# Performance work log

Hardware: AMD Instinct MI355X
Metric: run time of the kernel (lower is better)

The kernel has to match this reference:

```python
import jax, jax.numpy as jnp
import numpy as np
from jax.ops import segment_sum, segment_max

N = 50000          # nodes
E = 1_600_000      # edges (before self-loops)
IN = 16            # in_channels
F = 20             # N_features
H1 = 4             # heads in conv1
EDGE_DIM = 7
OUT = 3            # out_channels
NEG_SLOPE = 0.2


def setup_inputs() -> dict:
    key = jax.random.key(0)
    ks = jax.random.split(key, 24)
    g = lambda k, shape, fan: (jax.random.normal(k, shape, jnp.float32)
                               * (1.0 / np.sqrt(fan)))
    inp = {}
    inp["x"] = jax.random.normal(ks[0], (N, IN), jnp.float32)
    inp["edge_index"] = jax.random.randint(ks[1], (2, E), 0, N, jnp.int32)
    inp["edge_attr"] = jax.random.normal(ks[2], (E, EDGE_DIM), jnp.float32)
    # conv1: IN -> F, heads=H1, edge_dim=EDGE_DIM
    inp["W1"] = g(ks[3], (IN, H1 * F), IN)
    inp["att_src1"] = g(ks[4], (H1, F), F)
    inp["att_dst1"] = g(ks[5], (H1, F), F)
    inp["We1"] = g(ks[6], (EDGE_DIM, H1 * F), EDGE_DIM)
    inp["att_e1"] = g(ks[7], (H1, F), F)
    inp["b1"] = jnp.zeros((H1 * F,), jnp.float32)
    # conv2: (H1*F) -> F, heads=1, edge_dim=EDGE_DIM
    inp["W2"] = g(ks[8], (H1 * F, F), H1 * F)
    inp["att_src2"] = g(ks[9], (1, F), F)
    inp["att_dst2"] = g(ks[10], (1, F), F)
    inp["We2"] = g(ks[11], (EDGE_DIM, F), EDGE_DIM)
    inp["att_e2"] = g(ks[12], (1, F), F)
    inp["b2"] = jnp.zeros((F,), jnp.float32)
    # decoder: F -> 10 -> OUT
    inp["D1w"] = g(ks[13], (F, 10), F)
    inp["D1b"] = jnp.zeros((10,), jnp.float32)
    inp["D2w"] = g(ks[14], (10, OUT), 10)
    inp["D2b"] = jnp.zeros((OUT,), jnp.float32)
    return inp


def _gat_layer(x, src, dst, eattr, W, a_s, a_d, We, a_e, b, heads, fdim):
    """PyG GATConv (shared src/dst lin, add_self_loops already applied)."""
    n = x.shape[0]
    xh = (x @ W).reshape(n, heads, fdim)                  # [N,H,F]
    eh = (eattr @ We).reshape(-1, heads, fdim)            # [Ea,H,F]
    a_src = jnp.sum(xh * a_s, axis=-1)                    # [N,H]
    a_dst = jnp.sum(xh * a_d, axis=-1)                    # [N,H]
    a_edge = jnp.sum(eh * a_e, axis=-1)                   # [Ea,H]
    logits = a_src[src] + a_dst[dst] + a_edge             # [Ea,H]
    logits = jnp.where(logits >= 0, logits, NEG_SLOPE * logits)
    # segment softmax over destination node
    m = segment_max(logits, dst, num_segments=n)          # [N,H]
    ex = jnp.exp(logits - m[dst])
    denom = segment_sum(ex, dst, num_segments=n)          # [N,H]
    alpha = ex / (denom[dst] + 1e-16)                     # [Ea,H]
    msg = xh[src] * alpha[:, :, None]                     # [Ea,H,F]
    out = segment_sum(msg, dst, num_segments=n)           # [N,H,F]
    return out.reshape(n, heads * fdim) + b


def reference(x, edge_index, edge_attr, W1, att_src1, att_dst1, We1, att_e1,
              b1, W2, att_src2, att_dst2, We2, att_e2, b2, D1w, D1b, D2w, D2b):
    src, dst = edge_index[0], edge_index[1]
    # add self-loops with edge_attr fill_value='mean' (scatter-mean by dst)
    deg = segment_sum(jnp.ones((E,), jnp.float32), dst, num_segments=N)
    mean_attr = segment_sum(edge_attr, dst, num_segments=N) \
        / jnp.maximum(deg, 1.0)[:, None]
    loops = jnp.arange(N, dtype=src.dtype)
    src_a = jnp.concatenate([src, loops])
    dst_a = jnp.concatenate([dst, loops])
    eattr_a = jnp.concatenate([edge_attr, mean_attr], axis=0)
    # conv1 (heads=4, concat) -> elu  (dropouts are no-ops in eval)
    h = _gat_layer(x, src_a, dst_a, eattr_a, W1, att_src1, att_dst1,
                   We1, att_e1, b1, H1, F)
    h = jax.nn.elu(h)
    # conv2 (heads=1) -> elu
    h = _gat_layer(h, src_a, dst_a, eattr_a, W2, att_src2, att_dst2,
                   We2, att_e2, b2, 1, F)
    h = jax.nn.elu(h)
    # decoder MLP
    h = jax.nn.relu(h @ D1w + D1b)
    return h @ D2w + D2b
```

## Files before the change

### kernel.cpp

```cpp
#include <hip/hip_runtime.h>
#include <hip/hip_fp16.h>

constexpr int NN  = 50000;
constexpr int EEg = 1600000;
constexpr int IND = 16;
constexpr int FD  = 20;
constexpr int H1D = 4;
constexpr int ED  = 7;
constexpr int OUTD = 3;
constexpr int FP  = 24;

__device__ __forceinline__ float lrelu(float x) { return x >= 0.0f ? x : 0.2f * x; }
__device__ __forceinline__ float elu(float x)   { return x > 0.0f ? x : expm1f(x); }
__device__ __forceinline__ unsigned pack2(float a, float b) {
    __half2 h = __floats2half2_rn(a, b);
    return *(unsigned*)&h;
}
__device__ __forceinline__ float2 up2(unsigned w) {
    __half2 h = *(__half2*)&w;
    return __half22float2(h);
}

__global__ void k_deg(const int* __restrict__ ei, int* __restrict__ deg,
                      int* __restrict__ rank) {
    int e = blockIdx.x * blockDim.x + threadIdx.x;
    if (e >= EEg) return;
    rank[e] = atomicAdd(&deg[ei[EEg + e]], 1);
}

__global__ void k_ve(const float* __restrict__ We1, const float* __restrict__ ae1,
                     const float* __restrict__ We2, const float* __restrict__ ae2,
                     float* __restrict__ ve1, float* __restrict__ ve2) {
    int t = threadIdx.x;
    if (t < ED * H1D) {
        int d = t >> 2, h = t & 3;
        float s = 0.0f;
        for (int f = 0; f < FD; ++f) s += We1[d * (H1D * FD) + h * FD + f] * ae1[h * FD + f];
        ve1[t] = s;
    } else if (t < ED * H1D + ED) {
        int d = t - ED * H1D;
        float s = 0.0f;
        for (int f = 0; f < FD; ++f) s += We2[d * FD + f] * ae2[f];
        ve2[d] = s;
    }
}

__global__ void k_scanA(const int* __restrict__ deg, int* __restrict__ partial,
                        int* __restrict__ bsum) {
    __shared__ int sd[256];
    int t = threadIdx.x, i = blockIdx.x * 256 + t;
    int v = (i < NN) ? deg[i] : 0;
    sd[t] = v;
    __syncthreads();
    for (int off = 1; off < 256; off <<= 1) {
        int u = (t >= off) ? sd[t - off] : 0;
        __syncthreads();
        sd[t] += u;
        __syncthreads();
    }
    if (i < NN) partial[i] = sd[t] - v;
    if (t == 255) bsum[blockIdx.x] = sd[255];
}
__global__ void k_scanB(const int* __restrict__ bsum, int* __restrict__ boff, int nb) {
    __shared__ int sd[256];
    int t = threadIdx.x;
    int v = (t < nb) ? bsum[t] : 0;
    sd[t] = v;
    __syncthreads();
    for (int off = 1; off < 256; off <<= 1) {
        int u = (t >= off) ? sd[t - off] : 0;
        __syncthreads();
        sd[t] += u;
        __syncthreads();
    }
    if (t < nb) boff[t] = sd[t] - v;
}
__global__ void k_scanC(const int* __restrict__ partial, const int* __restrict__ boff,
                        int* __restrict__ row_off) {
    int i = blockIdx.x * 256 + threadIdx.x;
    if (i < NN) row_off[i] = partial[i] + boff[blockIdx.x];
    if (i == 0) row_off[NN] = EEg;
}

__global__ void k_scatter(const int* __restrict__ ei, const float* __restrict__ eattr,
                          const float* __restrict__ ve1, const float* __restrict__ ve2,
                          const int* __restrict__ row_off, const int* __restrict__ rank,
                          uint4* __restrict__ csr) {
    __shared__ float sv1[ED * H1D], sv2[ED];
    if (threadIdx.x < ED * H1D) sv1[threadIdx.x] = ve1[threadIdx.x];
    if (threadIdx.x < ED) sv2[threadIdx.x] = ve2[threadIdx.x];
    __syncthreads();
    int e = blockIdx.x * blockDim.x + threadIdx.x;
    if (e >= EEg) return;
    int src = ei[e], dst = ei[EEg + e];
    float a[ED];
#pragma unroll
    for (int d = 0; d < ED; ++d) a[d] = eattr[e * ED + d];
    float v0 = 0.f, v1 = 0.f, v2 = 0.f, v3 = 0.f, w2 = 0.f;
#pragma unroll
    for (int d = 0; d < ED; ++d) {
        v0 += a[d] * sv1[d * H1D + 0];
        v1 += a[d] * sv1[d * H1D + 1];
        v2 += a[d] * sv1[d * H1D + 2];
        v3 += a[d] * sv1[d * H1D + 3];
        w2 += a[d] * sv2[d];
    }
    int slot = row_off[dst] + rank[e];
    uint4 rec;
    rec.x = (unsigned)src;
    rec.y = pack2(v0, v1);
    rec.z = pack2(v2, v3);
    rec.w = pack2(w2, 0.0f);
    csr[slot] = rec;
}

__global__ void k_mean_self(const int* __restrict__ row_off, const uint4* __restrict__ csr,
                            float* __restrict__ a_e1s, float* __restrict__ a_e2s) {
    int n = blockIdx.x * blockDim.x + threadIdx.x;
    if (n >= NN) return;
    int beg = row_off[n], end = row_off[n + 1];
    float s0 = 0.f, s1 = 0.f, s2 = 0.f, s3 = 0.f, se = 0.f;
    for (int j = beg; j < end; ++j) {
        uint4 r = csr[j];
        float2 a01 = up2(r.y), a23 = up2(r.z), ap = up2(r.w);
        s0 += a01.x; s1 += a01.y; s2 += a23.x; s3 += a23.y; se += ap.x;
    }
    float inv = 1.0f / fmaxf((float)(end - beg), 1.0f);
    a_e1s[n * H1D + 0] = s0 * inv;
    a_e1s[n * H1D + 1] = s1 * inv;
    a_e1s[n * H1D + 2] = s2 * inv;
    a_e1s[n * H1D + 3] = s3 * inv;
    a_e2s[n] = se * inv;
}

__global__ void k_xh1attn1(const float* __restrict__ x, const float* __restrict__ W1,
                           const float* __restrict__ as, const float* __restrict__ ad,
                           __half* __restrict__ xh1h, float* __restrict__ a_src1,
                           float* __restrict__ a_dst1) {
    __shared__ float sW[IND * H1D * FD];
    for (int i = threadIdx.x; i < IND * H1D * FD; i += blockDim.x) sW[i] = W1[i];
    __syncthreads();
    int idx = blockIdx.x * blockDim.x + threadIdx.x;
    if (idx >= NN * H1D) return;
    int n = idx >> 2, h = idx & 3;
    float xr[IND];
    const float4* xp = (const float4*)&x[(size_t)n * IND];
#pragma unroll
    for (int q = 0; q < IND / 4; ++q) {
        float4 v = xp[q];
        xr[4 * q] = v.x; xr[4 * q + 1] = v.y; xr[4 * q + 2] = v.z; xr[4 * q + 3] = v.w;
    }
    float ss = 0.f, sd = 0.f;
    float o[FD];
#pragma unroll
    for (int f = 0; f < FD; ++f) {
        float s = 0.f;
#pragma unroll
        for (int k = 0; k < IND; ++k) s += xr[k] * sW[k * (H1D * FD) + h * FD + f];
        o[f] = s;
        ss += s * as[h * FD + f];
        sd += s * ad[h * FD + f];
    }
    uint4* xo = (uint4*)&xh1h[((size_t)n * H1D + h) * FP];
    xo[0] = make_uint4(pack2(o[0], o[1]), pack2(o[2], o[3]), pack2(o[4], o[5]), pack2(o[6], o[7]));
    xo[1] = make_uint4(pack2(o[8], o[9]), pack2(o[10], o[11]), pack2(o[12], o[13]), pack2(o[14], o[15]));
    xo[2] = make_uint4(pack2(o[16], o[17]), pack2(o[18], o[19]), 0u, 0u);
    a_src1[idx] = ss; a_dst1[idx] = sd;
}

#define FMA_PAYLOAD(ex, g0, g1, g2)                                     \
    {                                                                   \
        float2 f_;                                                      \
        f_ = up2(g0.x); acc[0] += (ex) * f_.x;  acc[1] += (ex) * f_.y;  \
        f_ = up2(g0.y); acc[2] += (ex) * f_.x;  acc[3] += (ex) * f_.y;  \
        f_ = up2(g0.z); acc[4] += (ex) * f_.x;  acc[5] += (ex) * f_.y;  \
        f_ = up2(g0.w); acc[6] += (ex) * f_.x;  acc[7] += (ex) * f_.y;  \
        f_ = up2(g1.x); acc[8] += (ex) * f_.x;  acc[9] += (ex) * f_.y;  \
        f_ = up2(g1.y); acc[10] += (ex) * f_.x; acc[11] += (ex) * f_.y; \
        f_ = up2(g1.z); acc[12] += (ex) * f_.x; acc[13] += (ex) * f_.y; \
        f_ = up2(g1.w); acc[14] += (ex) * f_.x; acc[15] += (ex) * f_.y; \
        f_ = up2(g2.x); acc[16] += (ex) * f_.x; acc[17] += (ex) * f_.y; \
        f_ = up2(g2.y); acc[18] += (ex) * f_.x; acc[19] += (ex) * f_.y; \
    }

__global__ __launch_bounds__(256) void k_conv1(
        const int* __restrict__ row_off, const uint4* __restrict__ csr,
        const float* __restrict__ a_src1, const float* __restrict__ a_dst1,
        const float* __restrict__ a_e1s, const __half* __restrict__ xh1h,
        const float* __restrict__ b1, float* __restrict__ h1) {
    int idx = blockIdx.x * 256 + threadIdx.x;
    int n = idx >> 4, low = idx & 15, h = low & 3, p = low >> 2;
    int beg = row_off[n], end = row_off[n + 1];
    float adst = a_dst1[n * H1D + h];
    float m, denom;
    float acc[FD];
#pragma unroll
    for (int f = 0; f < FD; ++f) acc[f] = 0.f;
    if (p == 0) {
        m = lrelu(a_src1[n * H1D + h] + adst + a_e1s[n * H1D + h]);
        denom = 1.0f;
        const uint4* xp = (const uint4*)&xh1h[((size_t)n * H1D + h) * FP];
        uint4 s0 = xp[0], s1 = xp[1];
        uint2 s2 = *(const uint2*)(xp + 2);
        FMA_PAYLOAD(1.0f, s0, s1, s2);
    } else {
        m = -1e30f; denom = 0.f;
    }
    int j = beg + p;
    uint4 r; float av; uint4 g0, g1; uint2 g2;
    if (j < end) {
        r = csr[j];
        int s = (int)r.x;
        av = a_src1[s * H1D + h];
        const uint4* xp = (const uint4*)&xh1h[((size_t)s * H1D + h) * FP];
        g0 = xp[0]; g1 = xp[1]; g2 = *(const uint2*)(xp + 2);
    }
    while (j < end) {
        int jn = j + 4;
        uint4 rn; float avn; uint4 n0, n1; uint2 n2;
        if (jn < end) {
            rn = csr[jn];
            int sn = (int)rn.x;
            avn = a_src1[sn * H1D + h];
            const uint4* xp = (const uint4*)&xh1h[((size_t)sn * H1D + h) * FP];
            n0 = xp[0]; n1 = xp[1]; n2 = *(const uint2*)(xp + 2);
        }
        unsigned wae = (h < 2) ? r.y : r.z;
        float2 aep = up2(wae);
        float ae = (h & 1) ? aep.y : aep.x;
        float l = lrelu(av + adst + ae);
        if (l > m) {
            float sc = __expf(m - l);
            denom *= sc;
#pragma unroll
            for (int f = 0; f < FD; ++f) acc[f] *= sc;
            m = l;
        }
        float ex = __expf(l - m);
        denom += ex;
        FMA_PAYLOAD(ex, g0, g1, g2);
        j = jn; r = rn; av = avn; g0 = n0; g1 = n1; g2 = n2;
    }
#pragma unroll
    for (int st = 4; st <= 8; st <<= 1) {
        float mo = __shfl_xor(m, st);
        float dno = __shfl_xor(denom, st);
        float M = fmaxf(m, mo);
        float ssf = __expf(m - M), sof = __expf(mo - M);
        denom = denom * ssf + dno * sof;
#pragma unroll
        for (int f = 0; f < FD; ++f) acc[f] = acc[f] * ssf + __shfl_xor(acc[f], st) * sof;
        m = M;
    }
    if (p) return;
    float inv = 1.0f / (denom + 1e-16f);
    float* ho = &h1[((size_t)n * H1D + h) * FD];
#pragma unroll
    for (int f = 0; f < FD; ++f) ho[f] = elu(acc[f] * inv + b1[h * FD + f]);
}

__global__ void k_xh2attn2(const float* __restrict__ h1, const float* __restrict__ W2,
                           const float* __restrict__ as, const float* __restrict__ ad,
                           __half* __restrict__ xh2h, float* __restrict__ a_src2,
                           float* __restrict__ a_dst2) {
    __shared__ float sW[H1D * FD * FD];
    for (int i = threadIdx.x; i < H1D * FD * FD; i += blockDim.x) sW[i] = W2[i];
    __syncthreads();
    int n = blockIdx.x * blockDim.x + threadIdx.x;
    if (n >= NN) return;
    float hr[H1D * FD];
    const float4* hp = (const float4*)&h1[(size_t)n * (H1D * FD)];
#pragma unroll
    for (int q = 0; q < (H1D * FD) / 4; ++q) {
        float4 v = hp[q];
        hr[4 * q] = v.x; hr[4 * q + 1] = v.y; hr[4 * q + 2] = v.z; hr[4 * q + 3] = v.w;
    }
    float ss = 0.f, sd = 0.f;
    float o[FD];
#pragma unroll
    for (int f = 0; f < FD; ++f) {
        float s = 0.f;
#pragma unroll
        for (int k = 0; k < H1D * FD; ++k) s += hr[k] * sW[k * FD + f];
        o[f] = s;
        ss += s * as[f];
        sd += s * ad[f];
    }
    uint4* xo = (uint4*)&xh2h[(size_t)n * FP];
    xo[0] = make_uint4(pack2(o[0], o[1]), pack2(o[2], o[3]), pack2(o[4], o[5]), pack2(o[6], o[7]));
    xo[1] = make_uint4(pack2(o[8], o[9]), pack2(o[10], o[11]), pack2(o[12], o[13]), pack2(o[14], o[15]));
    xo[2] = make_uint4(pack2(o[16], o[17]), pack2(o[18], o[19]), 0u, 0u);
    a_src2[n] = ss; a_dst2[n] = sd;
}

__global__ __launch_bounds__(256) void k_conv2dec(
        const int* __restrict__ row_off, const uint4* __restrict__ csr,
        const float* __restrict__ a_src2, const float* __restrict__ a_dst2,
        const float* __restrict__ a_e2s, const __half* __restrict__ xh2h,
        const float* __restrict__ b2, const float* __restrict__ D1w,
        const float* __restrict__ D1b, const float* __restrict__ D2w,
        const float* __restrict__ D2b, float* __restrict__ out) {
    __shared__ float sD1w[FD * 10], sD1b[10], sD2w[10 * OUTD], sD2b[OUTD], sb2[FD];
    for (int i = threadIdx.x; i < FD * 10; i += blockDim.x) sD1w[i] = D1w[i];
    if (threadIdx.x < 10) sD1b[threadIdx.x] = D1b[threadIdx.x];
    if (threadIdx.x < 10 * OUTD) sD2w[threadIdx.x] = D2w[threadIdx.x];
    if (threadIdx.x < OUTD) sD2b[threadIdx.x] = D2b[threadIdx.x];
    if (threadIdx.x < FD) sb2[threadIdx.x] = b2[threadIdx.x];
    __syncthreads();
    int idx = blockIdx.x * 256 + threadIdx.x;
    if (idx >= NN * 4) return;
    int n = idx >> 2, p = idx & 3;
    int beg = row_off[n], end = row_off[n + 1];
    float adst = a_dst2[n];
    float m, denom;
    float acc[FD];
#pragma unroll
    for (int f = 0; f < FD; ++f) acc[f] = 0.f;
    if (p == 0) {
        m = lrelu(a_src2[n] + adst + a_e2s[n]);
        denom = 1.0f;
        const uint4* xp = (const uint4*)&xh2h[(size_t)n * FP];
        uint4 s0 = xp[0], s1 = xp[1];
        uint2 s2 = *(const uint2*)(xp + 2);
        FMA_PAYLOAD(1.0f, s0, s1, s2);
    } else {
        m = -1e30f; denom = 0.f;
    }
    int j = beg + p;
    uint4 r; float av; uint4 g0, g1; uint2 g2;
    if (j < end) {
        r = csr[j];
        int s = (int)r.x;
        av = a_src2[s];
        const uint4* xp = (const uint4*)&xh2h[(size_t)s * FP];
        g0 = xp[0]; g1 = xp[1]; g2 = *(const uint2*)(xp + 2);
    }
    while (j < end) {
        int jn = j + 4;
        uint4 rn; float avn; uint4 n0, n1; uint2 n2;
        if (jn < end) {
            rn = csr[jn];
            int sn = (int)rn.x;
            avn = a_src2[sn];
            const uint4* xp = (const uint4*)&xh2h[(size_t)sn * FP];
            n0 = xp[0]; n1 = xp[1]; n2 = *(const uint2*)(xp + 2);
        }
        float l = lrelu(av + adst + up2(r.w).x);
        if (l > m) {
            float sc = __expf(m - l);
            denom *= sc;
#pragma unroll
            for (int f = 0; f < FD; ++f) acc[f] *= sc;
            m = l;
        }
        float ex = __expf(l - m);
        denom += ex;
        FMA_PAYLOAD(ex, g0, g1, g2);
        j = jn; r = rn; av = avn; g0 = n0; g1 = n1; g2 = n2;
    }
#pragma unroll
    for (int st = 1; st <= 2; st <<= 1) {
        float mo = __shfl_xor(m, st);
        float dno = __shfl_xor(denom, st);
        float M = fmaxf(m, mo);
        float ssf = __expf(m - M), sof = __expf(mo - M);
        denom = denom * ssf + dno * sof;
#pragma unroll
        for (int f = 0; f < FD; ++f) acc[f] = acc[f] * ssf + __shfl_xor(acc[f], st) * sof;
        m = M;
    }
    if (p) return;
    float inv = 1.0f / (denom + 1e-16f);
    float h2[FD];
#pragma unroll
    for (int f = 0; f < FD; ++f) h2[f] = elu(acc[f] * inv + sb2[f]);
    float o[OUTD];
#pragma unroll
    for (int k = 0; k < OUTD; ++k) o[k] = sD2b[k];
    for (int j2 = 0; j2 < 10; ++j2) {
        float hid = sD1b[j2];
#pragma unroll
        for (int f = 0; f < FD; ++f) hid += h2[f] * sD1w[f * 10 + j2];
        hid = fmaxf(hid, 0.0f);
#pragma unroll
        for (int k = 0; k < OUTD; ++k) o[k] += hid * sD2w[j2 * OUTD + k];
    }
#pragma unroll
    for (int k = 0; k < OUTD; ++k) out[n * OUTD + k] = o[k];
}

extern "C" void kernel_launch(void* const* d_in, const int* in_sizes, int n_in,
                              void* d_out, int out_size, void* d_ws, size_t ws_size,
                              hipStream_t stream) {
    const float* x     = (const float*)d_in[0];
    const int*   ei    = (const int*)d_in[1];
    const float* eattr = (const float*)d_in[2];
    const float* W1    = (const float*)d_in[3];
    const float* as1   = (const float*)d_in[4];
    const float* ad1   = (const float*)d_in[5];
    const float* We1   = (const float*)d_in[6];
    const float* ae1   = (const float*)d_in[7];
    const float* b1    = (const float*)d_in[8];
    const float* W2    = (const float*)d_in[9];
    const float* as2   = (const float*)d_in[10];
    const float* ad2   = (const float*)d_in[11];
    const float* We2   = (const float*)d_in[12];
    const float* ae2   = (const float*)d_in[13];
    const float* b2    = (const float*)d_in[14];
    const float* D1w   = (const float*)d_in[15];
    const float* D1b   = (const float*)d_in[16];
    const float* D2w   = (const float*)d_in[17];
    const float* D2b   = (const float*)d_in[18];
    float* out = (float*)d_out;

    float* w = (float*)d_ws;
    size_t o = 0;
    int*   deg = (int*)(w + o); o += NN;
    size_t zero_bytes = o * sizeof(float);
    int*   rank    = (int*)(w + o); o += EEg;
    int*   partial = (int*)(w + o); o += NN;
    int*   bsum    = (int*)(w + o); o += 256;
    int*   boff    = (int*)(w + o); o += 256;
    int*   row_off = (int*)(w + o); o += NN + 4;
    float* csr     = w + o; o += (size_t)EEg * 4;
    float* ve1     = w + o; o += 32;
    float* ve2     = w + o; o += 8;
    float* a_e1s   = w + o; o += (size_t)NN * H1D;
    float* a_e2s   = w + o; o += NN;
    float* a_src1  = w + o; o += (size_t)NN * H1D;
    float* a_dst1  = w + o; o += (size_t)NN * H1D;
    __half* xh1h   = (__half*)(w + o); o += (size_t)NN * H1D * FP / 2;
    float* h1      = w + o; o += (size_t)NN * H1D * FD;
    __half* xh2h   = (__half*)(w + o); o += (size_t)NN * FP / 2;
    float* a_src2  = w + o; o += NN;
    float* a_dst2  = w + o; o += NN;

    hipMemsetAsync(d_ws, 0, zero_bytes, stream);

    const int B = 256;
    auto cdiv = [](long a, long b) { return (int)((a + b - 1) / b); };
    const int NB = cdiv(NN, 256);

    k_deg<<<cdiv(EEg, B), B, 0, stream>>>(ei, deg, rank);
    k_ve<<<1, 64, 0, stream>>>(We1, ae1, We2, ae2, ve1, ve2);
    k_scanA<<<NB, 256, 0, stream>>>(deg, partial, bsum);
    k_scanB<<<1, 256, 0, stream>>>(bsum, boff, NB);
    k_scanC<<<NB, 256, 0, stream>>>(partial, boff, row_off);
    k_scatter<<<cdiv(EEg, B), B, 0, stream>>>(ei, eattr, ve1, ve2, row_off, rank,
                                              (uint4*)csr);
    k_mean_self<<<cdiv(NN, B), B, 0, stream>>>(row_off, (const uint4*)csr, a_e1s, a_e2s);
    k_xh1attn1<<<cdiv((long)NN * H1D, B), B, 0, stream>>>(x, W1, as1, ad1, xh1h, a_src1,
                                                          a_dst1);
    k_conv1<<<cdiv((long)NN * 16, 256), 256, 0, stream>>>(row_off, (const uint4*)csr,
                                                          a_src1, a_dst1, a_e1s, xh1h, b1,
                                                          h1);
    k_xh2attn2<<<cdiv(NN, B), B, 0, stream>>>(h1, W2, as2, ad2, xh2h, a_src2, a_dst2);
    k_conv2dec<<<cdiv((long)NN * 4, 256), 256, 0, stream>>>(row_off, (const uint4*)csr,
                                                            a_src2, a_dst2, a_e2s, xh2h,
                                                            b2, D1w, D1b, D2w, D2b, out);
}
```

Before: 283.1 us.

## Degree-sort nodes for load balance, stage edge attrs in LDS, shuffle CSR words

Builds a histogram of node degrees and a descending-degree permutation, then both conv kernels process nodes in that order so wavefronts hold nodes of similar degree and waste fewer lanes. The scatter kernel now stages edge attributes through shared memory with coalesced loads instead of strided per-thread loads. In conv1, each lane loads one 32-bit word of the CSR record and the source index and edge logit are shared with __shfl, instead of every lane loading the full uint4. The FMA macro is rewritten with explicit fmaf. This adds three small kernels plus the extra perm indirection, and output writes become scattered.

Result: slower. 522.0 us (+84.4%).

```diff
diff --git a/kernel.cpp b/kernel.cpp
--- a/kernel.cpp
+++ b/kernel.cpp
@@ -26,6 +26,33 @@
     int e = blockIdx.x * blockDim.x + threadIdx.x;
     if (e >= EEg) return;
     rank[e] = atomicAdd(&deg[ei[EEg + e]], 1);
+}
+
+__global__ void k_hist(const int* __restrict__ deg, int* __restrict__ hist) {
+    int n = blockIdx.x * blockDim.x + threadIdx.x;
+    if (n >= NN) return;
+    atomicAdd(&hist[min(deg[n], 255)], 1);
+}
+__global__ void k_hscan(const int* __restrict__ hist, int* __restrict__ hcur) {
+    __shared__ int sd[256];
+    int t = threadIdx.x;
+    int v = hist[255 - t];
+    sd[t] = v;
+    __syncthreads();
+    for (int off = 1; off < 256; off <<= 1) {
+        int u = (t >= off) ? sd[t - off] : 0;
+        __syncthreads();
+        sd[t] += u;
+        __syncthreads();
+    }
+    hcur[255 - t] = sd[t] - v;
+}
+__global__ void k_perm(const int* __restrict__ deg, int* __restrict__ hcur,
+                       int* __restrict__ perm) {
+    int n = blockIdx.x * blockDim.x + threadIdx.x;
+    if (n >= NN) return;
+    int slot = atomicAdd(&hcur[min(deg[n], 255)], 1);
+    perm[slot] = n;
 }
 
 __global__ void k_ve(const float* __restrict__ We1, const float* __restrict__ ae1,
@@ -82,28 +109,34 @@
     if (i == 0) row_off[NN] = EEg;
 }
 
-__global__ void k_scatter(const int* __restrict__ ei, const float* __restrict__ eattr,
-                          const float* __restrict__ ve1, const float* __restrict__ ve2,
-                          const int* __restrict__ row_off, const int* __restrict__ rank,
-                          uint4* __restrict__ csr) {
+__global__ __launch_bounds__(256) void k_scatter(
+        const int* __restrict__ ei, const float* __restrict__ eattr,
+        const float* __restrict__ ve1, const float* __restrict__ ve2,
+        const int* __restrict__ row_off, const int* __restrict__ rank,
+        uint4* __restrict__ csr) {
     __shared__ float sv1[ED * H1D], sv2[ED];
+    __shared__ float se[256 * ED];
     if (threadIdx.x < ED * H1D) sv1[threadIdx.x] = ve1[threadIdx.x];
     if (threadIdx.x < ED) sv2[threadIdx.x] = ve2[threadIdx.x];
-    __syncthreads();
-    int e = blockIdx.x * blockDim.x + threadIdx.x;
+    size_t gbase = (size_t)blockIdx.x * 256 * ED;
+    for (int i = threadIdx.x; i < 256 * ED; i += 256) {
+        size_t g = gbase + i;
+        if (g < (size_t)EEg * ED) se[i] = eattr[g];
+    }
+    __syncthreads();
+    int e = blockIdx.x * 256 + threadIdx.x;
     if (e >= EEg) return;
     int src = ei[e], dst = ei[EEg + e];
-    float a[ED];
-#pragma unroll
-    for (int d = 0; d < ED; ++d) a[d] = eattr[e * ED + d];
+    const float* a = &se[threadIdx.x * ED];
     float v0 = 0.f, v1 = 0.f, v2 = 0.f, v3 = 0.f, w2 = 0.f;
 #pragma unroll
     for (int d = 0; d < ED; ++d) {
-        v0 += a[d] * sv1[d * H1D + 0];
-        v1 += a[d] * sv1[d * H1D + 1];
-        v2 += a[d] * sv1[d * H1D + 2];
-        v3 += a[d] * sv1[d * H1D + 3];
-        w2 += a[d] * sv2[d];
+        float ad = a[d];
+        v0 += ad * sv1[d * H1D + 0];
+        v1 += ad * sv1[d * H1D + 1];
+        v2 += ad * sv1[d * H1D + 2];
+        v3 += ad * sv1[d * H1D + 3];
+        w2 += ad * sv2[d];
     }
     int slot = row_off[dst] + rank[e];
     uint4 rec;
@@ -168,28 +201,25 @@
     a_src1[idx] = ss; a_dst1[idx] = sd;
 }
 
-#define FMA_PAYLOAD(ex, g0, g1, g2)                                     \
-    {                                                                   \
-        float2 f_;                                                      \
-        f_ = up2(g0.x); acc[0] += (ex) * f_.x;  acc[1] += (ex) * f_.y;  \
-        f_ = up2(g0.y); acc[2] += (ex) * f_.x;  acc[3] += (ex) * f_.y;  \
-        f_ = up2(g0.z); acc[4] += (ex) * f_.x;  acc[5] += (ex) * f_.y;  \
-        f_ = up2(g0.w); acc[6] += (ex) * f_.x;  acc[7] += (ex) * f_.y;  \
-        f_ = up2(g1.x); acc[8] += (ex) * f_.x;  acc[9] += (ex) * f_.y;  \
-        f_ = up2(g1.y); acc[10] += (ex) * f_.x; acc[11] += (ex) * f_.y; \
-        f_ = up2(g1.z); acc[12] += (ex) * f_.x; acc[13] += (ex) * f_.y; \
-        f_ = up2(g1.w); acc[14] += (ex) * f_.x; acc[15] += (ex) * f_.y; \
-        f_ = up2(g2.x); acc[16] += (ex) * f_.x; acc[17] += (ex) * f_.y; \
-        f_ = up2(g2.y); acc[18] += (ex) * f_.x; acc[19] += (ex) * f_.y; \
-    }
+#define ACCH2(i, wrd) { __half2 h2_ = *(__half2*)&(wrd);               \
+    acc[i]     = fmaf(ex_, __low2float(h2_),  acc[i]);                 \
+    acc[i + 1] = fmaf(ex_, __high2float(h2_), acc[i + 1]); }
+#define FMA_PAYLOAD(ex, g0, g1, g2) { float ex_ = (ex);                \
+    ACCH2(0, g0.x) ACCH2(2, g0.y) ACCH2(4, g0.z) ACCH2(6, g0.w)        \
+    ACCH2(8, g1.x) ACCH2(10, g1.y) ACCH2(12, g1.z) ACCH2(14, g1.w)     \
+    ACCH2(16, g2.x) ACCH2(18, g2.y) }
 
 __global__ __launch_bounds__(256) void k_conv1(
-        const int* __restrict__ row_off, const uint4* __restrict__ csr,
-        const float* __restrict__ a_src1, const float* __restrict__ a_dst1,
-        const float* __restrict__ a_e1s, const __half* __restrict__ xh1h,
-        const float* __restrict__ b1, float* __restrict__ h1) {
+        const int* __restrict__ perm, const int* __restrict__ row_off,
+        const unsigned* __restrict__ cw, const float* __restrict__ a_src1,
+        const float* __restrict__ a_dst1, const float* __restrict__ a_e1s,
+        const __half* __restrict__ xh1h, const float* __restrict__ b1,
+        float* __restrict__ h1) {
     int idx = blockIdx.x * 256 + threadIdx.x;
-    int n = idx >> 4, low = idx & 15, h = low & 3, p = low >> 2;
+    int n = perm[idx >> 4];
+    int low = idx & 15, h = low & 3, p = low >> 2;
+    int lane = threadIdx.x & 63;
+    int lead = lane & ~3;
     int beg = row_off[n], end = row_off[n + 1];
     float adst = a_dst1[n * H1D + h];
     float m, denom;
@@ -207,26 +237,26 @@
         m = -1e30f; denom = 0.f;
     }
     int j = beg + p;
-    uint4 r; float av; uint4 g0, g1; uint2 g2;
+    unsigned wcur = 0u; int scur = 0; float av = 0.f; uint4 g0, g1; uint2 g2;
     if (j < end) {
-        r = csr[j];
-        int s = (int)r.x;
-        av = a_src1[s * H1D + h];
-        const uint4* xp = (const uint4*)&xh1h[((size_t)s * H1D + h) * FP];
+        wcur = cw[(size_t)j * 4 + h];
+        scur = (int)__shfl(wcur, lead);
+        av = a_src1[scur * H1D + h];
+        const uint4* xp = (const uint4*)&xh1h[((size_t)scur * H1D + h) * FP];
         g0 = xp[0]; g1 = xp[1]; g2 = *(const uint2*)(xp + 2);
     }
     while (j < end) {
         int jn = j + 4;
-        uint4 rn; float avn; uint4 n0, n1; uint2 n2;
+        unsigned wn = 0u; int sn = 0; float avn = 0.f; uint4 n0, n1; uint2 n2;
         if (jn < end) {
-            rn = csr[jn];
-            int sn = (int)rn.x;
+            wn = cw[(size_t)jn * 4 + h];
+            sn = (int)__shfl(wn, lead);
             avn = a_src1[sn * H1D + h];
             const uint4* xp = (const uint4*)&xh1h[((size_t)sn * H1D + h) * FP];
             n0 = xp[0]; n1 = xp[1]; n2 = *(const uint2*)(xp + 2);
         }
-        unsigned wae = (h < 2) ? r.y : r.z;
-        float2 aep = up2(wae);
+        unsigned aew = __shfl(wcur, lead + 1 + (h >> 1));
+        float2 aep = up2(aew);
         float ae = (h & 1) ? aep.y : aep.x;
         float l = lrelu(av + adst + ae);
         if (l > m) {
@@ -239,7 +269,7 @@
         float ex = __expf(l - m);
         denom += ex;
         FMA_PAYLOAD(ex, g0, g1, g2);
-        j = jn; r = rn; av = avn; g0 = n0; g1 = n1; g2 = n2;
+        j = jn; wcur = wn; scur = sn; av = avn; g0 = n0; g1 = n1; g2 = n2;
     }
 #pragma unroll
     for (int st = 4; st <= 8; st <<= 1) {
@@ -294,12 +324,13 @@
 }
 
 __global__ __launch_bounds__(256) void k_conv2dec(
-        const int* __restrict__ row_off, const uint4* __restrict__ csr,
-        const float* __restrict__ a_src2, const float* __restrict__ a_dst2,
-        const float* __restrict__ a_e2s, const __half* __restrict__ xh2h,
-        const float* __restrict__ b2, const float* __restrict__ D1w,
-        const float* __restrict__ D1b, const float* __restrict__ D2w,
-        const float* __restrict__ D2b, float* __restrict__ out) {
+        const int* __restrict__ perm, const int* __restrict__ row_off,
+        const uint4* __restrict__ csr, const float* __restrict__ a_src2,
+        const float* __restrict__ a_dst2, const float* __restrict__ a_e2s,
+        const __half* __restrict__ xh2h, const float* __restrict__ b2,
+        const float* __restrict__ D1w, const float* __restrict__ D1b,
+        const float* __restrict__ D2w, const float* __restrict__ D2b,
+        float* __restrict__ out) {
     __shared__ float sD1w[FD * 10], sD1b[10], sD2w[10 * OUTD], sD2b[OUTD], sb2[FD];
     for (int i = threadIdx.x; i < FD * 10; i += blockDim.x) sD1w[i] = D1w[i];
     if (threadIdx.x < 10) sD1b[threadIdx.x] = D1b[threadIdx.x];
@@ -309,7 +340,8 @@
     __syncthreads();
     int idx = blockIdx.x * 256 + threadIdx.x;
     if (idx >= NN * 4) return;
-    int n = idx >> 2, p = idx & 3;
+    int n = perm[idx >> 2];
+    int p = idx & 3;
     int beg = row_off[n], end = row_off[n + 1];
     float adst = a_dst2[n];
     float m, denom;
@@ -327,7 +359,7 @@
         m = -1e30f; denom = 0.f;
     }
     int j = beg + p;
-    uint4 r; float av; uint4 g0, g1; uint2 g2;
+    uint4 r; float av = 0.f; uint4 g0, g1; uint2 g2;
     if (j < end) {
         r = csr[j];
         int s = (int)r.x;
@@ -337,7 +369,7 @@
     }
     while (j < end) {
         int jn = j + 4;
-        uint4 rn; float avn; uint4 n0, n1; uint2 n2;
+        uint4 rn; float avn = 0.f; uint4 n0, n1; uint2 n2;
         if (jn < end) {
             rn = csr[jn];
             int sn = (int)rn.x;
@@ -415,8 +447,11 @@
 
     float* w = (float*)d_ws;
     size_t o = 0;
-    int*   deg = (int*)(w + o); o += NN;
+    int*   deg  = (int*)(w + o); o += NN;
+    int*   hist = (int*)(w + o); o += 256;
     size_t zero_bytes = o * sizeof(float);
+    int*   hcur    = (int*)(w + o); o += 256;
+    int*   perm    = (int*)(w + o); o += NN;
     int*   rank    = (int*)(w + o); o += EEg;
     int*   partial = (int*)(w + o); o += NN;
     int*   bsum    = (int*)(w + o); o += 256;
@@ -443,6 +478,9 @@
 
     k_deg<<<cdiv(EEg, B), B, 0, stream>>>(ei, deg, rank);
     k_ve<<<1, 64, 0, stream>>>(We1, ae1, We2, ae2, ve1, ve2);
+    k_hist<<<NB, 256, 0, stream>>>(deg, hist);
+    k_hscan<<<1, 256, 0, stream>>>(hist, hcur);
+    k_perm<<<NB, 256, 0, stream>>>(deg, hcur, perm);
     k_scanA<<<NB, 256, 0, stream>>>(deg, partial, bsum);
     k_scanB<<<1, 256, 0, stream>>>(bsum, boff, NB);
     k_scanC<<<NB, 256, 0, stream>>>(partial, boff, row_off);
@@ -451,11 +489,12 @@
     k_mean_self<<<cdiv(NN, B), B, 0, stream>>>(row_off, (const uint4*)csr, a_e1s, a_e2s);
     k_xh1attn1<<<cdiv((long)NN * H1D, B), B, 0, stream>>>(x, W1, as1, ad1, xh1h, a_src1,
                                                           a_dst1);
-    k_conv1<<<cdiv((long)NN * 16, 256), 256, 0, stream>>>(row_off, (const uint4*)csr,
-                                                          a_src1, a_dst1, a_e1s, xh1h, b1,
-                                                          h1);
+    k_conv1<<<cdiv((long)NN * 16, 256), 256, 0, stream>>>(perm, row_off,
+                                                          (const unsigned*)csr, a_src1,
+                                                          a_dst1, a_e1s, xh1h, b1, h1);
     k_xh2attn2<<<cdiv(NN, B), B, 0, stream>>>(h1, W2, as2, ad2, xh2h, a_src2, a_dst2);
-    k_conv2dec<<<cdiv((long)NN * 4, 256), 256, 0, stream>>>(row_off, (const uint4*)csr,
-                                                            a_src2, a_dst2, a_e2s, xh2h,
-                                                            b2, D1w, D1b, D2w, D2b, out);
-}
+    k_conv2dec<<<cdiv((long)NN * 4, 256), 256, 0, stream>>>(perm, row_off,
+                                                            (const uint4*)csr, a_src2,
+                                                            a_dst2, a_e2s, xh2h, b2,
+                                                            D1w, D1b, D2w, D2b, out);
+}
```

## Replace per-edge rank array with atomic cursor slots and stage edge attrs in LDS

Applied to the files above, without the earlier changes.

The degree kernel no longer writes a per-edge rank array. It becomes a grid-stride loop over a quarter-size grid, and the scatter kernel claims CSR slots with an atomicAdd on a per-node cursor initialised from the prefix scan. Edge attributes are loaded into shared memory with coalesced reads before the dot products, in place of strided per-thread loads. This removes a 6.4MB write and read of rank and improves coalescing, at the cost of a second round of contended atomics. Edge order within each CSR row becomes nondeterministic, which can change floating-point summation order.

Result: slower. 363.0 us (+28.2%).

```diff
diff --git a/kernel.cpp b/kernel.cpp
--- a/kernel.cpp
+++ b/kernel.cpp
@@ -21,11 +21,11 @@
     return __half22float2(h);
 }
 
-__global__ void k_deg(const int* __restrict__ ei, int* __restrict__ deg,
-                      int* __restrict__ rank) {
-    int e = blockIdx.x * blockDim.x + threadIdx.x;
-    if (e >= EEg) return;
-    rank[e] = atomicAdd(&deg[ei[EEg + e]], 1);
+__global__ void k_deg(const int* __restrict__ ei, int* __restrict__ deg) {
+    int i = blockIdx.x * blockDim.x + threadIdx.x;
+    int stride = gridDim.x * blockDim.x;
+    for (int e = i; e < EEg; e += stride)
+        atomicAdd(&deg[ei[EEg + e]], 1);
 }
 
 __global__ void k_ve(const float* __restrict__ We1, const float* __restrict__ ae1,
@@ -76,36 +76,45 @@
     if (t < nb) boff[t] = sd[t] - v;
 }
 __global__ void k_scanC(const int* __restrict__ partial, const int* __restrict__ boff,
-                        int* __restrict__ row_off) {
+                        int* __restrict__ row_off, int* __restrict__ cursor) {
     int i = blockIdx.x * 256 + threadIdx.x;
-    if (i < NN) row_off[i] = partial[i] + boff[blockIdx.x];
+    if (i < NN) {
+        int v = partial[i] + boff[blockIdx.x];
+        row_off[i] = v;
+        cursor[i] = v;
+    }
     if (i == 0) row_off[NN] = EEg;
 }
 
-__global__ void k_scatter(const int* __restrict__ ei, const float* __restrict__ eattr,
-                          const float* __restrict__ ve1, const float* __restrict__ ve2,
-                          const int* __restrict__ row_off, const int* __restrict__ rank,
-                          uint4* __restrict__ csr) {
+__global__ __launch_bounds__(256) void k_scatter(
+        const int* __restrict__ ei, const float* __restrict__ eattr,
+        const float* __restrict__ ve1, const float* __restrict__ ve2,
+        int* __restrict__ cursor, uint4* __restrict__ csr) {
     __shared__ float sv1[ED * H1D], sv2[ED];
+    __shared__ float se[256 * ED];
     if (threadIdx.x < ED * H1D) sv1[threadIdx.x] = ve1[threadIdx.x];
     if (threadIdx.x < ED) sv2[threadIdx.x] = ve2[threadIdx.x];
-    __syncthreads();
-    int e = blockIdx.x * blockDim.x + threadIdx.x;
+    size_t gbase = (size_t)blockIdx.x * 256 * ED;
+    for (int i = threadIdx.x; i < 256 * ED; i += 256) {
+        size_t g = gbase + i;
+        if (g < (size_t)EEg * ED) se[i] = eattr[g];
+    }
+    __syncthreads();
+    int e = blockIdx.x * 256 + threadIdx.x;
     if (e >= EEg) return;
     int src = ei[e], dst = ei[EEg + e];
-    float a[ED];
-#pragma unroll
-    for (int d = 0; d < ED; ++d) a[d] = eattr[e * ED + d];
+    const float* a = &se[threadIdx.x * ED];
     float v0 = 0.f, v1 = 0.f, v2 = 0.f, v3 = 0.f, w2 = 0.f;
 #pragma unroll
     for (int d = 0; d < ED; ++d) {
-        v0 += a[d] * sv1[d * H1D + 0];
-        v1 += a[d] * sv1[d * H1D + 1];
-        v2 += a[d] * sv1[d * H1D + 2];
-        v3 += a[d] * sv1[d * H1D + 3];
-        w2 += a[d] * sv2[d];
-    }
-    int slot = row_off[dst] + rank[e];
+        float ad = a[d];
+        v0 += ad * sv1[d * H1D + 0];
+        v1 += ad * sv1[d * H1D + 1];
+        v2 += ad * sv1[d * H1D + 2];
+        v3 += ad * sv1[d * H1D + 3];
+        w2 += ad * sv2[d];
+    }
+    int slot = atomicAdd(&cursor[dst], 1);
     uint4 rec;
     rec.x = (unsigned)src;
     rec.y = pack2(v0, v1);
@@ -417,7 +426,7 @@
     size_t o = 0;
     int*   deg = (int*)(w + o); o += NN;
     size_t zero_bytes = o * sizeof(float);
-    int*   rank    = (int*)(w + o); o += EEg;
+    int*   cursor  = (int*)(w + o); o += NN;
     int*   partial = (int*)(w + o); o += NN;
     int*   bsum    = (int*)(w + o); o += 256;
     int*   boff    = (int*)(w + o); o += 256;
@@ -441,13 +450,12 @@
     auto cdiv = [](long a, long b) { return (int)((a + b - 1) / b); };
     const int NB = cdiv(NN, 256);
 
-    k_deg<<<cdiv(EEg, B), B, 0, stream>>>(ei, deg, rank);
+    k_deg<<<cdiv(EEg / 4, B), B, 0, stream>>>(ei, deg);
     k_ve<<<1, 64, 0, stream>>>(We1, ae1, We2, ae2, ve1, ve2);
     k_scanA<<<NB, 256, 0, stream>>>(deg, partial, bsum);
     k_scanB<<<1, 256, 0, stream>>>(bsum, boff, NB);
-    k_scanC<<<NB, 256, 0, stream>>>(partial, boff, row_off);
-    k_scatter<<<cdiv(EEg, B), B, 0, stream>>>(ei, eattr, ve1, ve2, row_off, rank,
-                                              (uint4*)csr);
+    k_scanC<<<NB, 256, 0, stream>>>(partial, boff, row_off, cursor);
+    k_scatter<<<cdiv(EEg, B), B, 0, stream>>>(ei, eattr, ve1, ve2, cursor, (uint4*)csr);
     k_mean_self<<<cdiv(NN, B), B, 0, stream>>>(row_off, (const uint4*)csr, a_e1s, a_e2s);
     k_xh1attn1<<<cdiv((long)NN * H1D, B), B, 0, stream>>>(x, W1, as1, ad1, xh1h, a_src1,
                                                           a_dst1);
```
